# Kernel optimization log

Measured on AMD Instinct MI355X. Metric: run time of the kernel, lower is better.

Reference implementation:

```python
import jax, jax.numpy as jnp
import numpy as np

B, S, D, H = 2, 2048, 1024, 16
HD = D // H  # 64
EPS = 1e-8


def setup_inputs() -> dict:
    key = jax.random.key(0)
    ks = jax.random.split(key, 9)
    hidden_states = jax.random.normal(ks[0], (B, S, D), dtype=jnp.float32)
    # rotary tables: standard RoPE angles over half the head dim
    pos = jnp.arange(S, dtype=jnp.float32)[:, None]
    inv_freq = 1.0 / (10000.0 ** (jnp.arange(0, HD, 2, dtype=jnp.float32) / HD))  # [HD/2]
    ang = pos * inv_freq[None, :]  # [S, HD/2]
    sin = jnp.sin(ang)[None, None]  # [1,1,S,HD/2]
    cos = jnp.cos(ang)[None, None]
    s = 1.0 / np.sqrt(D)
    wq = jax.random.normal(ks[1], (D, D), dtype=jnp.float32) * s
    wk = jax.random.normal(ks[2], (D, D), dtype=jnp.float32) * s
    wv = jax.random.normal(ks[3], (D, D), dtype=jnp.float32) * s
    wo = jax.random.normal(ks[4], (D, D), dtype=jnp.float32) * s
    bo = jnp.zeros((D,), dtype=jnp.float32)
    scale = jnp.ones((D,), dtype=jnp.float32)
    return {"hidden_states": hidden_states, "sin": sin, "cos": cos,
            "wq": wq, "wk": wk, "wv": wv, "wo": wo, "bo": bo, "scale": scale}


def _heads(x):
    # [B,S,D] -> [B,H,S,HD]
    return x.reshape(B, S, H, HD).transpose(0, 2, 1, 3)


def _rotary(x, sin, cos):
    # interleaved RoPE: even/odd pairs
    x1, x2 = x[..., 0::2], x[..., 1::2]
    out = jnp.stack([x1 * cos - x2 * sin, x2 * cos + x1 * sin], axis=-1)
    return out.reshape(x.shape)


def reference(hidden_states, sin, cos, wq, wk, wv, wo, bo, scale):
    q = _rotary(_heads(hidden_states @ wq.T), sin, cos)
    k = _rotary(_heads(hidden_states @ wk.T), sin, cos)
    v = _rotary(_heads(hidden_states @ wv.T), sin, cos)
    scores = jnp.einsum("bhqd,bhkd->bhqk", q, k) / np.sqrt(HD)
    probs = jax.nn.softmax(scores, axis=-1)
    ctx = jnp.einsum("bhqk,bhkd->bhqd", probs, v)
    ctx = ctx.transpose(0, 2, 1, 3).reshape(B, S, D)
    out = ctx @ wo.T + bo
    x = out + hidden_states
    # RMSNorm: x / (||x||/sqrt(d) + eps) * scale
    rms = jnp.linalg.norm(x, axis=-1, keepdims=True) / np.sqrt(D)
    return scale * (x / (rms + EPS))
```

## Files before the change

kernel.cpp:

```cpp
#include <hip/hip_runtime.h>
#include <cmath>

#define BB 2
#define SS 2048
#define DD 1024
#define HH 16
#define HDIM 64
#define KDIM 1024
#define EPSF 1e-8f
#define QSCALE 0.18033688f

typedef __attribute__((ext_vector_type(8))) short bf16x8;
typedef __attribute__((ext_vector_type(4))) float f32x4;
typedef __attribute__((ext_vector_type(16))) float f32x16;

__device__ __forceinline__ ushort f2bf(float x) {
    unsigned u = __builtin_bit_cast(unsigned, x);
    u += 0x7FFFu + ((u >> 16) & 1u);
    return (ushort)(u >> 16);
}

__device__ __forceinline__ unsigned pack_bf16_trunc(float a, float b) {
    return __builtin_amdgcn_perm(__builtin_bit_cast(unsigned, b),
                                 __builtin_bit_cast(unsigned, a), 0x07060302u);
}

__device__ __forceinline__ float exp2_fast(float x) {
    float r;
    asm("v_exp_f32 %0, %1" : "=v"(r) : "v"(x));
    return r;
}

__device__ __forceinline__ void gload_lds16(const ushort* g, ushort* l) {
    __builtin_amdgcn_global_load_lds(
        (const __attribute__((address_space(1))) unsigned*)g,
        (__attribute__((address_space(3))) unsigned*)l, 16, 0, 0);
}

__global__ __launch_bounds__(256) void conv_all(
    const float* __restrict__ hs, const float* __restrict__ wq,
    const float* __restrict__ wk, const float* __restrict__ wv,
    const float* __restrict__ wo, ushort* __restrict__ dst)
{
    const int i = blockIdx.x * 256 + threadIdx.x;
    const int HS4 = (BB * SS * DD) / 4;
    const int W4 = (DD * DD) / 4;
    const float* src;
    int off;
    if (i < HS4) { src = hs; off = i; }
    else {
        const int j = i - HS4;
        const int seg = j / W4;
        off = j - seg * W4;
        src = (seg == 0) ? wq : (seg == 1) ? wk : (seg == 2) ? wv : wo;
    }
    const float4 v = ((const float4*)src)[off];
    ushort4 o;
    o.x = f2bf(v.x); o.y = f2bf(v.y); o.z = f2bf(v.z); o.w = f2bf(v.w);
    ((ushort4*)dst)[i] = o;
}

__global__ __launch_bounds__(256) void gemm_qkv_mfma(
    const ushort* __restrict__ A,
    const ushort* __restrict__ Wq, const ushort* __restrict__ Wk,
    const ushort* __restrict__ Wv,
    const float* __restrict__ sinp, const float* __restrict__ cosp,
    ushort* __restrict__ Qb, ushort* __restrict__ Kb, ushort* __restrict__ Vtb)
{
    const int cb = blockIdx.y;
    const int z = cb >> 3;
    const int col0 = (cb & 7) * 128;
    const ushort* W = (z == 0) ? Wq : (z == 1) ? Wk : Wv;
    ushort* O = (z == 0) ? Qb : (z == 1) ? Kb : Vtb;
    const int row0 = blockIdx.x * 128;
    const float qs = (z == 0) ? QSCALE : 1.0f;

    __shared__ __align__(16) ushort As[128 * 32];
    __shared__ __align__(16) ushort Bs[128 * 32];

    const int tid = threadIdx.x;
    const int w = tid >> 6, lane = tid & 63;
    const int quad = lane >> 4, l15 = lane & 15;
    const int m_off = (w >> 1) * 64, n_off = (w & 1) * 64;

    f32x4 acc[4][4] = {};

    for (int k0 = 0; k0 < KDIM; k0 += 32) {
#pragma unroll
        for (int it = 0; it < 2; ++it) {
            const int L = (it * 4 + w) * 64 + lane;
            const int r = L >> 2, c8 = (L & 3) * 8;
            gload_lds16(A + (size_t)(row0 + r) * KDIM + k0 + c8, &As[L * 8]);
            gload_lds16(W + (size_t)(col0 + r) * KDIM + k0 + c8, &Bs[L * 8]);
        }
        __syncthreads();
        bf16x8 af[4], bfr[4];
#pragma unroll
        for (int i = 0; i < 4; ++i) {
            af[i]  = *(const bf16x8*)&As[(m_off + i * 16 + l15) * 32 + quad * 8];
            bfr[i] = *(const bf16x8*)&Bs[(n_off + i * 16 + l15) * 32 + quad * 8];
        }
#pragma unroll
        for (int i = 0; i < 4; ++i)
#pragma unroll
            for (int j = 0; j < 4; ++j)
                acc[i][j] = __builtin_amdgcn_mfma_f32_16x16x32_bf16(
                    af[i], bfr[j], acc[i][j], 0, 0, 0);
        __syncthreads();
    }

    const int b = (row0 + m_off) / SS;
#pragma unroll
    for (int mi = 0; mi < 4; ++mi) {
        const int mrow = row0 + m_off + mi * 16 + quad * 4;
#pragma unroll
        for (int ni = 0; ni < 4; ++ni) {
            const int c = col0 + n_off + ni * 16 + l15;
            const int h = c >> 6, e = c & 63;
            const int bh = b * HH + h;
            float outv[4];
#pragma unroll
            for (int r = 0; r < 4; ++r) {
                const int s = (mrow + r) & (SS - 1);
                const float sv = sinp[s * (HDIM / 2) + (e >> 1)];
                const float cv = cosp[s * (HDIM / 2) + (e >> 1)];
                const float v = acc[mi][ni][r];
                const float vp = __shfl_xor(v, 1);
                outv[r] = ((l15 & 1) ? (v * cv + vp * sv) : (v * cv - vp * sv)) * qs;
            }
            if (z < 2) {
#pragma unroll
                for (int r = 0; r < 4; ++r) {
                    const int s = (mrow + r) & (SS - 1);
                    const ushort mine = f2bf(outv[r]);
                    const ushort part = (ushort)__shfl_xor((int)mine, 1);
                    if (!(l15 & 1))
                        *(unsigned*)(O + ((size_t)(bh * SS + s)) * HDIM + e) =
                            (unsigned)mine | ((unsigned)part << 16);
                }
            } else {
                ushort4 pk;
                pk.x = f2bf(outv[0]); pk.y = f2bf(outv[1]);
                pk.z = f2bf(outv[2]); pk.w = f2bf(outv[3]);
                const int s0 = mrow & (SS - 1);
                *(ushort4*)(O + ((size_t)(bh * HDIM + e)) * SS + s0) = pk;
            }
        }
    }
}

__global__ __launch_bounds__(256, 2) void attn_mfma(
    const ushort* __restrict__ Qb, const ushort* __restrict__ Kb,
    const ushort* __restrict__ Vtb, ushort* __restrict__ ctx)
{
    const int wg  = blockIdx.x;
    const int lin = (wg & 7) * 64 + (wg >> 3);
    const int bh   = lin >> 4;
    const int qblk = lin & 15;
    const int b = bh / HH, h = bh % HH;
    const int q0 = qblk * 128;
    const int tid = threadIdx.x;
    const int w = tid >> 6;
    const int lane = tid & 63;
    const int l31 = lane & 31;
    const int g = lane >> 5;
    const int strip = w >> 1;
    const int phase = w & 1;

    __shared__ __align__(16) ushort kvb[2][2][2][64][32];

    const ushort* Qh = Qb  + (size_t)bh * SS * HDIM;
    const ushort* Kh = Kb  + (size_t)bh * SS * HDIM;
    const ushort* Vh = Vtb + (size_t)bh * HDIM * SS;

    const int qrowA = q0 + strip * 64 + l31;
    const int qrowB = qrowA + 32;
    bf16x8 qf[2][4];
#pragma unroll
    for (int ks = 0; ks < 4; ++ks) {
        qf[0][ks] = *(const bf16x8*)(Qh + (size_t)qrowA * HDIM + ks * 16 + g * 8);
        qf[1][ks] = *(const bf16x8*)(Qh + (size_t)qrowB * HDIM + ks * 16 + g * 8);
    }

    f32x16 cacc[2][2] = {};
    float ls0a = 0.f, ls0b = 0.f, ls1a = 0.f, ls1b = 0.f;

    const int lr = lane >> 2;
    const int c16 = lane & 3;
    const int lc = c16 * 8;
    const int swc = (c16 ^ ((lr >> 1) & 3)) * 8;
    const int srow = w * 16 + lr;
    const int rsw = (l31 >> 1) & 3;

    uint4 rk0, rk1, rv0, rv1;

#define LOAD_STAGE(K0)                                                        \
    do {                                                                      \
        const ushort* Kp = Kh + (size_t)((K0) + srow) * HDIM + lc;            \
        const ushort* Vp = Vh + (size_t)srow * SS + (K0) + lc;                \
        rk0 = *(const uint4*)(Kp);                                            \
        rk1 = *(const uint4*)(Kp + 32);                                       \
        rv0 = *(const uint4*)(Vp);                                            \
        rv1 = *(const uint4*)(Vp + 32);                                       \
    } while (0)

#define WRITE_STAGE(bufi)                                                     \
    do {                                                                      \
        *(uint4*)&kvb[bufi][0][0][srow][swc] = rk0;                           \
        *(uint4*)&kvb[bufi][0][1][srow][swc] = rk1;                           \
        *(uint4*)&kvb[bufi][1][0][srow][swc] = rv0;                           \
        *(uint4*)&kvb[bufi][1][1][srow][swc] = rv1;                           \
    } while (0)

    const int NT = SS / 64;

    LOAD_STAGE(0);
    WRITE_STAGE(0);
    LOAD_STAGE(64);

    for (int t = 0; t < NT; ++t) {
        __syncthreads();
        const int cur = t & 1;

        bf16x8 kf[4];
#pragma unroll
        for (int ks = 0; ks < 4; ++ks)
            kf[ks] = *(const bf16x8*)&kvb[cur][0][ks >> 1]
                [phase * 32 + l31][(((ks & 1) * 2 + g) ^ rsw) * 8];

        if (t + 1 < NT) WRITE_STAGE(cur ^ 1);
        if (t + 2 < NT) LOAD_STAGE((t + 2) * 64);

        f32x16 sacc0 = {}, sacc1 = {};
        __builtin_amdgcn_s_setprio(1);
#pragma unroll
        for (int ks = 0; ks < 4; ++ks) {
            sacc0 = __builtin_amdgcn_mfma_f32_32x32x16_bf16(
                kf[ks], qf[0][ks], sacc0, 0, 0, 0);
            sacc1 = __builtin_amdgcn_mfma_f32_32x32x16_bf16(
                kf[ks], qf[1][ks], sacc1, 0, 0, 0);
        }
        __builtin_amdgcn_s_setprio(0);

        unsigned pk[2][8];
#pragma unroll
        for (int i = 0; i < 8; ++i) {
            const float pa0 = exp2_fast(sacc0[2 * i]);
            const float pb0 = exp2_fast(sacc0[2 * i + 1]);
            const float pa1 = exp2_fast(sacc1[2 * i]);
            const float pb1 = exp2_fast(sacc1[2 * i + 1]);
            if (i & 1) { ls0b += pa0 + pb0; ls1b += pa1 + pb1; }
            else       { ls0a += pa0 + pb0; ls1a += pa1 + pb1; }
            pk[0][i] = pack_bf16_trunc(pa0, pb0);
            pk[1][i] = pack_bf16_trunc(pa1, pb1);
        }

#pragma unroll
        for (int ks = 0; ks < 2; ++ks) {
            const int bq = ks * 4;
            unsigned a00 = pk[0][bq + 0], a01 = pk[0][bq + 1];
            unsigned b00 = pk[0][bq + 2], b01 = pk[0][bq + 3];
            unsigned a10 = pk[1][bq + 0], a11 = pk[1][bq + 1];
            unsigned b10 = pk[1][bq + 2], b11 = pk[1][bq + 3];
            asm("v_permlane32_swap_b32 %0, %1" : "+v"(a00), "+v"(b00));
            asm("v_permlane32_swap_b32 %0, %1" : "+v"(a01), "+v"(b01));
            asm("v_permlane32_swap_b32 %0, %1" : "+v"(a10), "+v"(b10));
            asm("v_permlane32_swap_b32 %0, %1" : "+v"(a11), "+v"(b11));
            union { unsigned u[4]; bf16x8 v; } pf0, pf1;
            pf0.u[0] = a00; pf0.u[1] = a01; pf0.u[2] = b00; pf0.u[3] = b01;
            pf1.u[0] = a10; pf1.u[1] = a11; pf1.u[2] = b10; pf1.u[3] = b11;
            __builtin_amdgcn_s_setprio(1);
#pragma unroll
            for (int dt = 0; dt < 2; ++dt) {
                const bf16x8 vf = *(const bf16x8*)&kvb[cur][1][phase]
                    [dt * 32 + l31][((ks * 2 + g) ^ rsw) * 8];
                cacc[0][dt] = __builtin_amdgcn_mfma_f32_32x32x16_bf16(
                    vf, pf0.v, cacc[0][dt], 0, 0, 0);
                cacc[1][dt] = __builtin_amdgcn_mfma_f32_32x32x16_bf16(
                    vf, pf1.v, cacc[1][dt], 0, 0, 0);
            }
            __builtin_amdgcn_s_setprio(0);
        }
    }

    float lsq[2];
    lsq[0] = ls0a + ls0b;
    lsq[1] = ls1a + ls1b;
    lsq[0] += __shfl_xor(lsq[0], 32);
    lsq[1] += __shfl_xor(lsq[1], 32);

    float* mlds = (float*)kvb;
    const int mbase = strip * 2112 + lane * 33;
#pragma unroll
    for (int qs = 0; qs < 2; ++qs) {
        __syncthreads();
        if (phase == 1) {
#pragma unroll
            for (int dt = 0; dt < 2; ++dt)
#pragma unroll
                for (int i = 0; i < 16; ++i)
                    mlds[mbase + dt * 16 + i] = cacc[qs][dt][i];
            mlds[mbase + 32] = lsq[qs];
        }
        __syncthreads();
        if (phase == 0) {
            f32x16 cf[2];
#pragma unroll
            for (int dt = 0; dt < 2; ++dt)
#pragma unroll
                for (int i = 0; i < 16; ++i)
                    cf[dt][i] = cacc[qs][dt][i] + mlds[mbase + dt * 16 + i];
            const float inv = 1.f / (lsq[qs] + mlds[mbase + 32]);

            const int qrow = (qs == 0) ? qrowA : qrowB;
            const size_t obase = ((size_t)(b * SS + qrow)) * DD + h * HDIM;
#pragma unroll
            for (int dt = 0; dt < 2; ++dt)
#pragma unroll
                for (int tt = 0; tt < 4; ++tt) {
                    ushort4 o;
                    o.x = f2bf(cf[dt][tt * 4 + 0] * inv);
                    o.y = f2bf(cf[dt][tt * 4 + 1] * inv);
                    o.z = f2bf(cf[dt][tt * 4 + 2] * inv);
                    o.w = f2bf(cf[dt][tt * 4 + 3] * inv);
                    *(ushort4*)(ctx + obase + dt * 32 + tt * 8 + g * 4) = o;
                }
        }
    }
#undef LOAD_STAGE
#undef WRITE_STAGE
}

__global__ __launch_bounds__(256) void gemm_out_mfma(
    const ushort* __restrict__ A, const ushort* __restrict__ W,
    const float* __restrict__ bias, float* __restrict__ Out)
{
    const int row0 = blockIdx.x * 128;
    const int col0 = blockIdx.y * 64;

    __shared__ __align__(16) ushort As[128 * 32];
    __shared__ __align__(16) ushort Bs[64 * 32];

    const int tid = threadIdx.x;
    const int w = tid >> 6, lane = tid & 63;
    const int quad = lane >> 4, l15 = lane & 15;
    const int m_off = (w >> 1) * 64, n_off = (w & 1) * 32;

    f32x4 acc[4][2] = {};

    for (int k0 = 0; k0 < KDIM; k0 += 32) {
#pragma unroll
        for (int it = 0; it < 2; ++it) {
            const int L = (it * 4 + w) * 64 + lane;
            const int r = L >> 2, c8 = (L & 3) * 8;
            gload_lds16(A + (size_t)(row0 + r) * KDIM + k0 + c8, &As[L * 8]);
        }
        {
            const int L = w * 64 + lane;
            const int r = L >> 2, c8 = (L & 3) * 8;
            gload_lds16(W + (size_t)(col0 + r) * KDIM + k0 + c8, &Bs[L * 8]);
        }
        __syncthreads();
        bf16x8 af[4], bfr[2];
#pragma unroll
        for (int i = 0; i < 4; ++i)
            af[i] = *(const bf16x8*)&As[(m_off + i * 16 + l15) * 32 + quad * 8];
#pragma unroll
        for (int j = 0; j < 2; ++j)
            bfr[j] = *(const bf16x8*)&Bs[(n_off + j * 16 + l15) * 32 + quad * 8];
#pragma unroll
        for (int i = 0; i < 4; ++i)
#pragma unroll
            for (int j = 0; j < 2; ++j)
                acc[i][j] = __builtin_amdgcn_mfma_f32_16x16x32_bf16(
                    af[i], bfr[j], acc[i][j], 0, 0, 0);
        __syncthreads();
    }

#pragma unroll
    for (int mi = 0; mi < 4; ++mi) {
        const int mrow = row0 + m_off + mi * 16 + quad * 4;
#pragma unroll
        for (int ni = 0; ni < 2; ++ni) {
            const int c = col0 + n_off + ni * 16 + l15;
            const float bv = bias[c];
#pragma unroll
            for (int r = 0; r < 4; ++r)
                Out[(size_t)(mrow + r) * DD + c] = acc[mi][ni][r] + bv;
        }
    }
}

__global__ __launch_bounds__(256) void resid_rmsnorm(
    const float* __restrict__ proj, const float* __restrict__ hs,
    const float* __restrict__ scale, float* __restrict__ out)
{
    const int t = blockIdx.x;
    const int tid = threadIdx.x;
    const size_t base = (size_t)t * DD + tid * 4;

    const float4 p4 = *(const float4*)(proj + base);
    const float4 h4 = *(const float4*)(hs + base);
    float x0 = p4.x + h4.x, x1 = p4.y + h4.y, x2 = p4.z + h4.z, x3 = p4.w + h4.w;
    float ss = x0 * x0 + x1 * x1 + x2 * x2 + x3 * x3;

#pragma unroll
    for (int off = 1; off < 64; off <<= 1) ss += __shfl_xor(ss, off);

    __shared__ float wsum[4];
    if ((tid & 63) == 0) wsum[tid >> 6] = ss;
    __syncthreads();
    const float total = wsum[0] + wsum[1] + wsum[2] + wsum[3];
    const float inv = 1.f / (sqrtf(total * (1.f / DD)) + EPSF);

    const float4 s4 = *(const float4*)(scale + tid * 4);
    float4 o;
    o.x = s4.x * x0 * inv;
    o.y = s4.y * x1 * inv;
    o.z = s4.z * x2 * inv;
    o.w = s4.w * x3 * inv;
    *(float4*)(out + base) = o;
}

extern "C" void kernel_launch(void* const* d_in, const int* in_sizes, int n_in,
                              void* d_out, int out_size, void* d_ws, size_t ws_size,
                              hipStream_t stream) {
    const float* hs    = (const float*)d_in[0];
    const float* sinp  = (const float*)d_in[1];
    const float* cosp  = (const float*)d_in[2];
    const float* wq    = (const float*)d_in[3];
    const float* wk    = (const float*)d_in[4];
    const float* wv    = (const float*)d_in[5];
    const float* wo    = (const float*)d_in[6];
    const float* bo    = (const float*)d_in[7];
    const float* scale = (const float*)d_in[8];
    float* out = (float*)d_out;

    unsigned char* wsb = (unsigned char*)d_ws;
    const size_t MAT = (size_t)BB * SS * DD;
    const size_t WN  = (size_t)DD * DD;
    ushort* Abf = (ushort*)wsb;
    ushort* Wqb = Abf + MAT;
    ushort* Wkb = Wqb + WN;
    ushort* Wvb = Wkb + WN;
    ushort* Wob = Wvb + WN;
    ushort* Qb  = Wob + WN;
    ushort* Kb  = Qb + MAT;
    ushort* Vtb = Kb + MAT;
    ushort* ctxb = Vtb + MAT;
    float* proj = (float*)(ctxb + MAT);

    const int nconv4 = (int)((MAT + 4 * WN) / 4);
    conv_all<<<dim3(nconv4 / 256), 256, 0, stream>>>(hs, wq, wk, wv, wo, Abf);

    gemm_qkv_mfma<<<dim3(32, 24), 256, 0, stream>>>(Abf, Wqb, Wkb, Wvb,
                                                    sinp, cosp, Qb, Kb, Vtb);
    attn_mfma<<<dim3(512), 256, 0, stream>>>(Qb, Kb, Vtb, ctxb);
    gemm_out_mfma<<<dim3(32, 16), 256, 0, stream>>>(ctxb, Wob, bo, proj);
    resid_rmsnorm<<<dim3(BB * SS), 256, 0, stream>>>(proj, hs, scale, out);
}
```

Baseline: 195.3 us.

## Widen QKV GEMM K-tile with XOR-swizzled LDS and remap workgroups for XCD locality

The QKV projection GEMM now stages a 64-wide K slice per iteration instead of 32. This halves the number of barrier pairs, and an XOR swizzle on the LDS column index avoids bank conflicts on the fragment reads. Both GEMMs switch to a 1D grid with a remapped block index, so that consecutive blocks on the same XCD share weight and activation tiles in L2. The larger LDS footprint (32 KB per block) may reduce occupancy.

```diff
diff --git a/kernel.cpp b/kernel.cpp
--- a/kernel.cpp
+++ b/kernel.cpp
@@ -67,45 +67,54 @@
     const float* __restrict__ sinp, const float* __restrict__ cosp,
     ushort* __restrict__ Qb, ushort* __restrict__ Kb, ushort* __restrict__ Vtb)
 {
-    const int cb = blockIdx.y;
+    const int wg = blockIdx.x;
+    const int lin = (wg & 7) * 96 + (wg >> 3);
+    const int cb = lin >> 5;
+    const int row0 = (lin & 31) * 128;
     const int z = cb >> 3;
     const int col0 = (cb & 7) * 128;
     const ushort* W = (z == 0) ? Wq : (z == 1) ? Wk : Wv;
     ushort* O = (z == 0) ? Qb : (z == 1) ? Kb : Vtb;
-    const int row0 = blockIdx.x * 128;
     const float qs = (z == 0) ? QSCALE : 1.0f;
 
-    __shared__ __align__(16) ushort As[128 * 32];
-    __shared__ __align__(16) ushort Bs[128 * 32];
+    __shared__ __align__(16) ushort As[128 * 64];
+    __shared__ __align__(16) ushort Bs[128 * 64];
 
     const int tid = threadIdx.x;
     const int w = tid >> 6, lane = tid & 63;
     const int quad = lane >> 4, l15 = lane & 15;
     const int m_off = (w >> 1) * 64, n_off = (w & 1) * 64;
+    const int rxor = l15 & 7;
 
     f32x4 acc[4][4] = {};
 
-    for (int k0 = 0; k0 < KDIM; k0 += 32) {
-#pragma unroll
-        for (int it = 0; it < 2; ++it) {
-            const int L = (it * 4 + w) * 64 + lane;
-            const int r = L >> 2, c8 = (L & 3) * 8;
-            gload_lds16(A + (size_t)(row0 + r) * KDIM + k0 + c8, &As[L * 8]);
-            gload_lds16(W + (size_t)(col0 + r) * KDIM + k0 + c8, &Bs[L * 8]);
-        }
-        __syncthreads();
-        bf16x8 af[4], bfr[4];
-#pragma unroll
-        for (int i = 0; i < 4; ++i) {
-            af[i]  = *(const bf16x8*)&As[(m_off + i * 16 + l15) * 32 + quad * 8];
-            bfr[i] = *(const bf16x8*)&Bs[(n_off + i * 16 + l15) * 32 + quad * 8];
-        }
-#pragma unroll
-        for (int i = 0; i < 4; ++i)
-#pragma unroll
-            for (int j = 0; j < 4; ++j)
-                acc[i][j] = __builtin_amdgcn_mfma_f32_16x16x32_bf16(
-                    af[i], bfr[j], acc[i][j], 0, 0, 0);
+    for (int k0 = 0; k0 < KDIM; k0 += 64) {
+#pragma unroll
+        for (int r = 0; r < 4; ++r) {
+            const int id = r * 256 + tid;
+            const int row = id >> 3, cc = id & 7;
+            const int sc = (cc ^ (row & 7)) * 8;
+            gload_lds16(A + (size_t)(row0 + row) * KDIM + k0 + sc, &As[id * 8]);
+            gload_lds16(W + (size_t)(col0 + row) * KDIM + k0 + sc, &Bs[id * 8]);
+        }
+        __syncthreads();
+#pragma unroll
+        for (int ks2 = 0; ks2 < 2; ++ks2) {
+            bf16x8 af[4], bfr[4];
+#pragma unroll
+            for (int i = 0; i < 4; ++i) {
+                const int ar = m_off + i * 16 + l15;
+                const int br = n_off + i * 16 + l15;
+                af[i]  = *(const bf16x8*)&As[ar * 64 + (((ks2 * 4 + quad) ^ rxor)) * 8];
+                bfr[i] = *(const bf16x8*)&Bs[br * 64 + (((ks2 * 4 + quad) ^ rxor)) * 8];
+            }
+#pragma unroll
+            for (int i = 0; i < 4; ++i)
+#pragma unroll
+                for (int j = 0; j < 4; ++j)
+                    acc[i][j] = __builtin_amdgcn_mfma_f32_16x16x32_bf16(
+                        af[i], bfr[j], acc[i][j], 0, 0, 0);
+        }
         __syncthreads();
     }
 
@@ -335,8 +344,10 @@
     const ushort* __restrict__ A, const ushort* __restrict__ W,
     const float* __restrict__ bias, float* __restrict__ Out)
 {
-    const int row0 = blockIdx.x * 128;
-    const int col0 = blockIdx.y * 64;
+    const int wg = blockIdx.x;
+    const int lin = (wg & 7) * 64 + (wg >> 3);
+    const int row0 = (lin & 31) * 128;
+    const int col0 = (lin >> 5) * 64;
 
     __shared__ __align__(16) ushort As[128 * 32];
     __shared__ __align__(16) ushort Bs[64 * 32];
@@ -453,9 +464,9 @@
     const int nconv4 = (int)((MAT + 4 * WN) / 4);
     conv_all<<<dim3(nconv4 / 256), 256, 0, stream>>>(hs, wq, wk, wv, wo, Abf);
 
-    gemm_qkv_mfma<<<dim3(32, 24), 256, 0, stream>>>(Abf, Wqb, Wkb, Wvb,
-                                                    sinp, cosp, Qb, Kb, Vtb);
+    gemm_qkv_mfma<<<dim3(768), 256, 0, stream>>>(Abf, Wqb, Wkb, Wvb,
+                                                 sinp, cosp, Qb, Kb, Vtb);
     attn_mfma<<<dim3(512), 256, 0, stream>>>(Qb, Kb, Vtb, ctxb);
-    gemm_out_mfma<<<dim3(32, 16), 256, 0, stream>>>(ctxb, Wob, bo, proj);
+    gemm_out_mfma<<<dim3(512), 256, 0, stream>>>(ctxb, Wob, bo, proj);
     resid_rmsnorm<<<dim3(BB * SS), 256, 0, stream>>>(proj, hs, scale, out);
 }
```

New measurement: 214.9 us. 10.0% more time.
